# Kernel optimization log

Hardware: AMD Instinct MI355X
Metric: run time of the kernel (lower is better)

Reference implementation:

```python
import jax, jax.numpy as jnp
import numpy as np

N = 100_000      # nodes
E = 3_200_000    # edges (avg degree 32)
G = 1024         # graphs in batch
IN_FEAT = 6
H_FEAT = 64
NUM_TARGETS = 2
NEG_SLOPE = 0.01


def setup_inputs() -> dict:
    key = jax.random.key(0)
    ks = jax.random.split(key, 9)
    x = jax.random.normal(ks[0], (N, IN_FEAT), jnp.float32)
    edge_index = jax.random.randint(ks[1], (2, E), 0, N, dtype=jnp.int64)
    batch = jnp.sort(jax.random.randint(ks[2], (N,), 0, G, dtype=jnp.int64))
    W1 = jax.random.normal(ks[3], (IN_FEAT, H_FEAT), jnp.float32) / np.sqrt(IN_FEAT)
    b1 = jnp.zeros((H_FEAT,), jnp.float32)
    W2 = jax.random.normal(ks[4], (H_FEAT, H_FEAT // 2), jnp.float32) / np.sqrt(H_FEAT)
    b2 = jnp.zeros((H_FEAT // 2,), jnp.float32)
    Wlin = jax.random.normal(ks[5], (H_FEAT // 2, NUM_TARGETS), jnp.float32) / np.sqrt(H_FEAT // 2)
    blin = jnp.zeros((NUM_TARGETS,), jnp.float32)
    return {"x": x, "edge_index": edge_index, "batch": batch,
            "W1": W1, "b1": b1, "W2": W2, "b2": b2, "Wlin": Wlin, "blin": blin}


def _gcn_conv(x, W, b, src, dst, dis):
    # GCNConv: linear transform, then symmetric-normalized scatter-add.
    h = x @ W                                   # [N, out]
    norm = dis[src] * dis[dst]                  # [E+N]
    msg = h[src] * norm[:, None]                # gather + scale
    out = jax.ops.segment_sum(msg, dst, num_segments=N)
    return out + b


def reference(x, edge_index, batch, W1, b1, W2, b2, Wlin, blin):
    loop = jnp.arange(N, dtype=edge_index.dtype)
    src = jnp.concatenate([edge_index[0], loop])   # add self-loops
    dst = jnp.concatenate([edge_index[1], loop])
    deg = jax.ops.segment_sum(jnp.ones_like(dst, dtype=x.dtype), dst, num_segments=N)
    dis = jax.lax.rsqrt(jnp.maximum(deg, 1.0))     # deg >= 1 via self-loops

    h = jax.nn.leaky_relu(_gcn_conv(x, W1, b1, src, dst, dis), NEG_SLOPE)
    h = jax.nn.leaky_relu(_gcn_conv(h, W2, b2, src, dst, dis), NEG_SLOPE)

    # global_mean_pool over graph ids
    sums = jax.ops.segment_sum(h, batch, num_segments=G)              # [G, 32]
    cnt = jax.ops.segment_sum(jnp.ones((N,), h.dtype), batch, num_segments=G)
    pooled = sums / jnp.maximum(cnt, 1.0)[:, None]

    # dropout(p=0.5) is identity in eval mode
    return pooled @ Wlin + blin                                        # [G, 2]
```

## Files before the change

### kernel.cpp

```cpp
#include <hip/hip_runtime.h>


#define N_NODES 100000
#define N_EDGES 3200000
#define N_GRAPHS 1024
#define IN_F 6
#define H1 64
#define H2 32
#define SLOPE 0.01f

#define NBIN 400
#define BIN_N 250
#define CAP2 8704
#define CAP2R 10752

#define SEG 8192
#define NSEGB ((N_EDGES + SEG - 1) / SEG)

typedef _Float16 f16;
typedef _Float16 h2 __attribute__((ext_vector_type(2)));
typedef float f2 __attribute__((ext_vector_type(2)));
typedef int  iv4 __attribute__((ext_vector_type(4)));

static __device__ __forceinline__ float lrelu(float v) {
    return v > 0.0f ? v : SLOPE * v;
}

static __device__ __forceinline__ h2 uph(unsigned w) {
    union { unsigned u; h2 h; } cv; cv.u = w;
    return cv.h;
}

static __device__ __forceinline__ void upk8(unsigned w, f2& lo, f2& hi) {
    lo = __builtin_amdgcn_cvt_pk_f32_fp8((int)w, false);
    hi = __builtin_amdgcn_cvt_pk_f32_fp8((int)w, true);
}

static __device__ __forceinline__ unsigned pk8(float a, float b, float c, float d) {
    int v = __builtin_amdgcn_cvt_pk_fp8_f32(a, b, 0, false);
    v = __builtin_amdgcn_cvt_pk_fp8_f32(c, d, v, true);
    return (unsigned)v;
}

__global__ void k_init(float* __restrict__ gz, int* __restrict__ bz,
                       unsigned* __restrict__ t2z, f16* __restrict__ sxz) {
    int i = blockIdx.x * blockDim.x + threadIdx.x;
    if (i < N_GRAPHS * H2 + N_GRAPHS) gz[i] = 0.0f;
    if (i < NBIN + 16) bz[i] = 0;
    if (i < 8) t2z[i] = 0u;
    if (i < 8) sxz[i] = (f16)0.0f;
}

__global__ void k_bin400(const int* __restrict__ src, const int* __restrict__ dst,
                         int* __restrict__ bcur2, unsigned* __restrict__ benc2) {
    __shared__ int hist[NBIN];
    __shared__ int lscan[NBIN];
    __shared__ int lcur[NBIN];
    __shared__ int gbase[NBIN];
    __shared__ int scn[512];
    __shared__ unsigned codes[SEG];
    __shared__ unsigned short bslot[SEG];
    int tid = threadIdx.x;
    for (int i = tid; i < NBIN; i += 256) hist[i] = 0;
    __syncthreads();
    int e0 = blockIdx.x * SEG;
    int e1 = e0 + SEG; if (e1 > N_EDGES) e1 = N_EDGES;
    int cnt = e1 - e0;
    const iv4* d4 = (const iv4*)dst;
    const iv4* s4 = (const iv4*)src;
    int i40 = e0 >> 2, i41 = e1 >> 2;
    for (int i4 = i40 + tid; i4 < i41; i4 += 256) {
        iv4 v = __builtin_nontemporal_load(d4 + i4);
        atomicAdd(&hist[v.x / BIN_N], 1);
        atomicAdd(&hist[v.y / BIN_N], 1);
        atomicAdd(&hist[v.z / BIN_N], 1);
        atomicAdd(&hist[v.w / BIN_N], 1);
    }
    __syncthreads();
    scn[tid]       = (tid < NBIN) ? hist[tid] : 0;
    scn[tid + 256] = (tid + 256 < NBIN) ? hist[tid + 256] : 0;
    __syncthreads();
    for (int off = 1; off < 512; off <<= 1) {
        int v0 = (tid >= off) ? scn[tid - off] : 0;
        int v1 = (tid + 256 >= off) ? scn[tid + 256 - off] : 0;
        __syncthreads();
        scn[tid] += v0;
        scn[tid + 256] += v1;
        __syncthreads();
    }
    if (tid < NBIN) {
        int h = hist[tid];
        int ls = scn[tid] - h;
        lscan[tid] = ls;
        lcur[tid] = ls;
        gbase[tid] = h ? atomicAdd(&bcur2[tid], h) : 0;
        for (int j = ls; j < ls + h; ++j) bslot[j] = (unsigned short)tid;
    }
    if (tid + 256 < NBIN) {
        int t = tid + 256;
        int h = hist[t];
        int ls = scn[t] - h;
        lscan[t] = ls;
        lcur[t] = ls;
        gbase[t] = h ? atomicAdd(&bcur2[t], h) : 0;
        for (int j = ls; j < ls + h; ++j) bslot[j] = (unsigned short)t;
    }
    __syncthreads();
    for (int i4 = i40 + tid; i4 < i41; i4 += 256) {
        iv4 dv = __builtin_nontemporal_load(d4 + i4);
        iv4 sv = __builtin_nontemporal_load(s4 + i4);
        int b, p;
        b = dv.x / BIN_N; p = atomicAdd(&lcur[b], 1);
        codes[p] = ((unsigned)sv.x << 8) | (unsigned)(dv.x - b * BIN_N);
        b = dv.y / BIN_N; p = atomicAdd(&lcur[b], 1);
        codes[p] = ((unsigned)sv.y << 8) | (unsigned)(dv.y - b * BIN_N);
        b = dv.z / BIN_N; p = atomicAdd(&lcur[b], 1);
        codes[p] = ((unsigned)sv.z << 8) | (unsigned)(dv.z - b * BIN_N);
        b = dv.w / BIN_N; p = atomicAdd(&lcur[b], 1);
        codes[p] = ((unsigned)sv.w << 8) | (unsigned)(dv.w - b * BIN_N);
    }
    __syncthreads();
    for (int slot = tid; slot < cnt; slot += 256) {
        int b = bslot[slot];
        int g = gbase[b] + (slot - lscan[b]);
        benc2[(long long)b * CAP2 + g] = codes[slot];
    }
}

__global__ void k_sort(const unsigned* __restrict__ benc2, const int* __restrict__ bcur2,
                       const float* __restrict__ x,
                       int* __restrict__ csr, int* __restrict__ obeg, int* __restrict__ oend,
                       float* __restrict__ dis, f16* __restrict__ sx) {
    __shared__ int hist[256];
    __shared__ int scn[256];
    __shared__ int lcur[256];
    int bin = blockIdx.x;
    int tid = threadIdx.x;
    hist[tid] = 0;
    __syncthreads();
    int cnt = bcur2[bin];
    const unsigned* p = benc2 + (long long)bin * CAP2;
    for (int i = tid; i < cnt; i += 256)
        atomicAdd(&hist[p[i] & 0xFFu], 1);
    __syncthreads();
    int deg = hist[tid];
    int pad = (deg + 7) & ~7;
    scn[tid] = pad;
    __syncthreads();
    for (int off = 1; off < 256; off <<= 1) {
        int v = 0;
        if (tid >= off) v = scn[tid - off];
        __syncthreads();
        if (tid >= off) scn[tid] += v;
        __syncthreads();
    }
    int excl = scn[tid] - pad;
    int gbase = bin * CAP2R;
    lcur[tid] = gbase + excl;
    if (tid < BIN_N) {
        int n = bin * BIN_N + tid;
        obeg[n] = gbase + excl;
        oend[n] = gbase + excl + pad;
        float dn = rsqrtf((float)(deg + 1));
        dis[n] = dn;
#pragma unroll
        for (int j = 0; j < IN_F; ++j)
            sx[n * 8 + j] = (f16)(x[n * IN_F + j] * dn);
        sx[n * 8 + 6] = (f16)0.0f;
        sx[n * 8 + 7] = (f16)0.0f;
    }
    __syncthreads();
    for (int i = tid; i < cnt; i += 256) {
        unsigned c = p[i];
        int pos = atomicAdd(&lcur[c & 0xFFu], 1);
        csr[pos] = (int)(c >> 8);
    }
    __syncthreads();
    if (tid < BIN_N) {
        int end = gbase + excl + pad;
        for (int j = lcur[tid]; j < end; ++j) csr[j] = N_NODES;
    }
}

__global__ void k_l1(const unsigned* __restrict__ sxu, const int* __restrict__ obeg,
                     const int* __restrict__ oend, const int* __restrict__ csr,
                     const float* __restrict__ W1, const float* __restrict__ b1,
                     const float* __restrict__ W2, const float* __restrict__ dis,
                     unsigned* __restrict__ t2) {
    __shared__ float sW1[IN_F * H1];
    __shared__ float sb1[H1];
    __shared__ float sW2[H1 * H2];
    __shared__ float sagg[64][9];
    __shared__ float sh1[64][H1 + 1];
    __shared__ float sdis[64];
    int tid = threadIdx.x;
    for (int i = tid; i < IN_F * H1; i += 256) sW1[i] = W1[i];
    if (tid < H1) sb1[tid] = b1[tid];
    for (int i = tid; i < H1 * H2; i += 256) sW2[i] = W2[i];
    int loc = tid >> 2;
    int f = tid & 3;
    int n = blockIdx.x * 64 + loc;
    bool ok = n < N_NODES;
    if (ok) {
        h2 acc = uph(sxu[(n << 2) + f]);
        int b = obeg[n], e = oend[n];
        for (int j = b; j < e; j += 8) {
            const iv4* p = (const iv4*)(csr + j);
            iv4 ia = p[0], ib = p[1];
            unsigned w[8];
            w[0] = sxu[(ia.x << 2) + f]; w[1] = sxu[(ia.y << 2) + f];
            w[2] = sxu[(ia.z << 2) + f]; w[3] = sxu[(ia.w << 2) + f];
            w[4] = sxu[(ib.x << 2) + f]; w[5] = sxu[(ib.y << 2) + f];
            w[6] = sxu[(ib.z << 2) + f]; w[7] = sxu[(ib.w << 2) + f];
            h2 s01 = uph(w[0]) + uph(w[1]);
            h2 s23 = uph(w[2]) + uph(w[3]);
            h2 s45 = uph(w[4]) + uph(w[5]);
            h2 s67 = uph(w[6]) + uph(w[7]);
            acc += (s01 + s23) + (s45 + s67);
        }
        sagg[loc][2*f]   = (float)acc.x;
        sagg[loc][2*f+1] = (float)acc.y;
        if (f == 0) sdis[loc] = dis[n];
    }
    __syncthreads();
    float dn = sdis[loc];
#pragma unroll
    for (int q = 0; q < 16; ++q) {
        int k = (f << 4) + q;
        float s = 0.0f;
#pragma unroll
        for (int j = 0; j < IN_F; ++j) s += sagg[loc][j] * sW1[j * H1 + k];
        sh1[loc][k] = lrelu(s * dn + sb1[k]);
    }
    __syncthreads();
    float r[8];
#pragma unroll
    for (int q = 0; q < 8; ++q) {
        int f2i = (f << 3) + q;
        float s = 0.0f;
#pragma unroll
        for (int k = 0; k < H1; ++k) s += sh1[loc][k] * sW2[k * H2 + f2i];
        r[q] = s * dn;
    }
    if (ok) {
        uint2 pk;
        pk.x = pk8(r[0], r[1], r[2], r[3]);
        pk.y = pk8(r[4], r[5], r[6], r[7]);
        *((uint2*)(t2 + n * 8 + f * 2)) = pk;
    }
}

__global__ void k_gather2(const unsigned* __restrict__ t2u, const int* __restrict__ obeg,
                          const int* __restrict__ oend, const int* __restrict__ csr,
                          const float* __restrict__ dis, const float* __restrict__ b2,
                          const int* __restrict__ batch,
                          float* __restrict__ gsum, float* __restrict__ gcnt) {
    __shared__ float sv[32][H2];
    __shared__ int sg[32];
    int idx = blockIdx.x * blockDim.x + threadIdx.x;
    int n = idx >> 3;
    int f = idx & 7;
    f2 a01, a23;
    upk8(t2u[(n << 3) + f], a01, a23);
    int b = obeg[n], e = oend[n];
    int j = b;
    for (; j + 16 <= e; j += 16) {
        const iv4* p = (const iv4*)(csr + j);
        iv4 ia = p[0], ib = p[1], ic = p[2], id = p[3];
        unsigned w[16];
        w[0]  = t2u[(ia.x << 3) + f]; w[1]  = t2u[(ia.y << 3) + f];
        w[2]  = t2u[(ia.z << 3) + f]; w[3]  = t2u[(ia.w << 3) + f];
        w[4]  = t2u[(ib.x << 3) + f]; w[5]  = t2u[(ib.y << 3) + f];
        w[6]  = t2u[(ib.z << 3) + f]; w[7]  = t2u[(ib.w << 3) + f];
        w[8]  = t2u[(ic.x << 3) + f]; w[9]  = t2u[(ic.y << 3) + f];
        w[10] = t2u[(ic.z << 3) + f]; w[11] = t2u[(ic.w << 3) + f];
        w[12] = t2u[(id.x << 3) + f]; w[13] = t2u[(id.y << 3) + f];
        w[14] = t2u[(id.z << 3) + f]; w[15] = t2u[(id.w << 3) + f];
#pragma unroll
        for (int q = 0; q < 16; ++q) {
            f2 lo, hi;
            upk8(w[q], lo, hi);
            a01 += lo;
            a23 += hi;
        }
    }
    if (j < e) {
        const iv4* p = (const iv4*)(csr + j);
        iv4 ia = p[0], ib = p[1];
        unsigned w[8];
        w[0] = t2u[(ia.x << 3) + f]; w[1] = t2u[(ia.y << 3) + f];
        w[2] = t2u[(ia.z << 3) + f]; w[3] = t2u[(ia.w << 3) + f];
        w[4] = t2u[(ib.x << 3) + f]; w[5] = t2u[(ib.y << 3) + f];
        w[6] = t2u[(ib.z << 3) + f]; w[7] = t2u[(ib.w << 3) + f];
#pragma unroll
        for (int q = 0; q < 8; ++q) {
            f2 lo, hi;
            upk8(w[q], lo, hi);
            a01 += lo;
            a23 += hi;
        }
    }
    float dn = dis[n];
    float v0 = lrelu(a01.x * dn + b2[4*f]);
    float v1 = lrelu(a01.y * dn + b2[4*f+1]);
    float v2 = lrelu(a23.x * dn + b2[4*f+2]);
    float v3 = lrelu(a23.y * dn + b2[4*f+3]);
    int g = batch[n];
    int loc = threadIdx.x >> 3;
    sv[loc][4*f]   = v0;
    sv[loc][4*f+1] = v1;
    sv[loc][4*f+2] = v2;
    sv[loc][4*f+3] = v3;
    if (f == 0) sg[loc] = g;
    __syncthreads();
    bool leader = true;
    for (int l = 0; l < loc; ++l) leader &= (sg[l] != g);
    if (leader) {
        float s0 = v0, s1 = v1, s2 = v2, s3 = v3;
        float c = 1.0f;
        for (int l = loc + 1; l < 32; ++l)
            if (sg[l] == g) {
                s0 += sv[l][4*f];   s1 += sv[l][4*f+1];
                s2 += sv[l][4*f+2]; s3 += sv[l][4*f+3];
                c += 1.0f;
            }
        atomicAdd(&gsum[g * H2 + 4*f],     s0);
        atomicAdd(&gsum[g * H2 + 4*f + 1], s1);
        atomicAdd(&gsum[g * H2 + 4*f + 2], s2);
        atomicAdd(&gsum[g * H2 + 4*f + 3], s3);
        if (f == 0) atomicAdd(&gcnt[g], c);
    }
}

__global__ void k_final(const float* __restrict__ gsum, const float* __restrict__ gcnt,
                        const float* __restrict__ Wlin, const float* __restrict__ blin,
                        float* __restrict__ out) {
    int idx = blockIdx.x * blockDim.x + threadIdx.x;
    if (idx >= N_GRAPHS * 2) return;
    int g = idx >> 1;
    int t = idx & 1;
    float inv = 1.0f / fmaxf(gcnt[g], 1.0f);
    float s = blin[t];
#pragma unroll
    for (int ff = 0; ff < H2; ++ff)
        s += gsum[g * H2 + ff] * inv * Wlin[ff * 2 + t];
    out[idx] = s;
}

static inline int cdiv(long long a, int b) { return (int)((a + b - 1) / b); }

extern "C" void kernel_launch(void* const* d_in, const int* in_sizes, int n_in,
                              void* d_out, int out_size, void* d_ws, size_t ws_size,
                              hipStream_t stream) {
    const float* x    = (const float*)d_in[0];
    const int*   ei   = (const int*)d_in[1];
    const int*   batch= (const int*)d_in[2];
    const float* W1   = (const float*)d_in[3];
    const float* b1   = (const float*)d_in[4];
    const float* W2   = (const float*)d_in[5];
    const float* b2   = (const float*)d_in[6];
    const float* Wlin = (const float*)d_in[7];
    const float* blin = (const float*)d_in[8];
    float* out = (float*)d_out;

    const int* src = ei;
    const int* dst = ei + N_EDGES;

    unsigned* t2 = (unsigned*)d_ws;
    f16*   sx   = (f16*)(t2 + 8LL * (N_NODES + 1));
    float* dis  = (float*)(sx + 8LL * (N_NODES + 1));
    float* gsum = dis + N_NODES;
    float* gcnt = gsum + (long long)N_GRAPHS * H2;
    size_t ioff = ((size_t)(gcnt + N_GRAPHS) + 15) & ~(size_t)15;
    int*  bcur2   = (int*)ioff;
    int*  obeg    = bcur2 + NBIN + 16;
    int*  oend    = obeg + N_NODES;
    unsigned* benc2 = (unsigned*)(oend + N_NODES);
    int*  csr      = (int*)(benc2 + (long long)NBIN * CAP2);

    const int B = 256;

    k_init<<<cdiv(N_GRAPHS * H2 + N_GRAPHS, B), B, 0, stream>>>(
        gsum, bcur2, t2 + 8LL * N_NODES, sx + 8LL * N_NODES);

    k_bin400<<<NSEGB, B, 0, stream>>>(src, dst, bcur2, benc2);
    k_sort<<<NBIN, B, 0, stream>>>(benc2, bcur2, x, csr, obeg, oend, dis, sx);

    k_l1<<<cdiv(N_NODES, 64), B, 0, stream>>>((const unsigned*)sx, obeg, oend, csr,
                                              W1, b1, W2, dis, t2);
    k_gather2<<<cdiv((long long)N_NODES * 8, B), B, 0, stream>>>(
        (const unsigned*)t2, obeg, oend, csr, dis, b2, batch, gsum, gcnt);
    k_final<<<cdiv(N_GRAPHS * 2, B), B, 0, stream>>>(gsum, gcnt, Wlin, blin, out);
}
```

Before: 128.9 us.

## Partition bin buffers per XCD to localize atomics and writes

The binning kernel now reads the hardware XCC id and keeps a separate set of bin counters and bin buffers for each of the 8 XCDs. This avoids cross-XCD contention on the global atomic counters and keeps the scattered writes local to one die. The sort kernel then walks all 8 sub-buckets for its bin. The cost is more, smaller segments to read, and the per-XCD capacity of 3072 could overflow if the distribution of blocks across XCDs is skewed.

After: 118.2 us. -8.3%, faster.

```diff
diff --git a/kernel.cpp b/kernel.cpp
--- a/kernel.cpp
+++ b/kernel.cpp
@@ -11,11 +11,14 @@
 
 #define NBIN 400
 #define BIN_N 250
-#define CAP2 8704
+#define NXCD 8
+#define CAP2X 3072
 #define CAP2R 10752
 
 #define SEG 8192
 #define NSEGB ((N_EDGES + SEG - 1) / SEG)
+
+#define XCC_ID_REG 14356
 
 typedef _Float16 f16;
 typedef _Float16 h2 __attribute__((ext_vector_type(2)));
@@ -46,7 +49,7 @@
                        unsigned* __restrict__ t2z, f16* __restrict__ sxz) {
     int i = blockIdx.x * blockDim.x + threadIdx.x;
     if (i < N_GRAPHS * H2 + N_GRAPHS) gz[i] = 0.0f;
-    if (i < NBIN + 16) bz[i] = 0;
+    if (i < NXCD * NBIN + 16) bz[i] = 0;
     if (i < 8) t2z[i] = 0u;
     if (i < 8) sxz[i] = (f16)0.0f;
 }
@@ -61,6 +64,9 @@
     __shared__ unsigned codes[SEG];
     __shared__ unsigned short bslot[SEG];
     int tid = threadIdx.x;
+    int xcd = __builtin_amdgcn_s_getreg(XCC_ID_REG) & (NXCD - 1);
+    int* mycur = bcur2 + xcd * NBIN;
+    unsigned* myenc = benc2 + (long long)xcd * NBIN * CAP2X;
     for (int i = tid; i < NBIN; i += 256) hist[i] = 0;
     __syncthreads();
     int e0 = blockIdx.x * SEG;
@@ -93,7 +99,7 @@
         int ls = scn[tid] - h;
         lscan[tid] = ls;
         lcur[tid] = ls;
-        gbase[tid] = h ? atomicAdd(&bcur2[tid], h) : 0;
+        gbase[tid] = h ? atomicAdd(&mycur[tid], h) : 0;
         for (int j = ls; j < ls + h; ++j) bslot[j] = (unsigned short)tid;
     }
     if (tid + 256 < NBIN) {
@@ -102,7 +108,7 @@
         int ls = scn[t] - h;
         lscan[t] = ls;
         lcur[t] = ls;
-        gbase[t] = h ? atomicAdd(&bcur2[t], h) : 0;
+        gbase[t] = h ? atomicAdd(&mycur[t], h) : 0;
         for (int j = ls; j < ls + h; ++j) bslot[j] = (unsigned short)t;
     }
     __syncthreads();
@@ -123,7 +129,7 @@
     for (int slot = tid; slot < cnt; slot += 256) {
         int b = bslot[slot];
         int g = gbase[b] + (slot - lscan[b]);
-        benc2[(long long)b * CAP2 + g] = codes[slot];
+        myenc[(long long)b * CAP2X + g] = codes[slot];
     }
 }
 
@@ -138,10 +144,12 @@
     int tid = threadIdx.x;
     hist[tid] = 0;
     __syncthreads();
-    int cnt = bcur2[bin];
-    const unsigned* p = benc2 + (long long)bin * CAP2;
-    for (int i = tid; i < cnt; i += 256)
-        atomicAdd(&hist[p[i] & 0xFFu], 1);
+    for (int xc = 0; xc < NXCD; ++xc) {
+        int cnt = bcur2[xc * NBIN + bin];
+        const unsigned* p = benc2 + ((long long)xc * NBIN + bin) * CAP2X;
+        for (int i = tid; i < cnt; i += 256)
+            atomicAdd(&hist[p[i] & 0xFFu], 1);
+    }
     __syncthreads();
     int deg = hist[tid];
     int pad = (deg + 7) & ~7;
@@ -170,10 +178,14 @@
         sx[n * 8 + 7] = (f16)0.0f;
     }
     __syncthreads();
-    for (int i = tid; i < cnt; i += 256) {
-        unsigned c = p[i];
-        int pos = atomicAdd(&lcur[c & 0xFFu], 1);
-        csr[pos] = (int)(c >> 8);
+    for (int xc = 0; xc < NXCD; ++xc) {
+        int cnt = bcur2[xc * NBIN + bin];
+        const unsigned* p = benc2 + ((long long)xc * NBIN + bin) * CAP2X;
+        for (int i = tid; i < cnt; i += 256) {
+            unsigned c = p[i];
+            int pos = atomicAdd(&lcur[c & 0xFFu], 1);
+            csr[pos] = (int)(c >> 8);
+        }
     }
     __syncthreads();
     if (tid < BIN_N) {
@@ -371,12 +383,13 @@
     float* dis  = (float*)(sx + 8LL * (N_NODES + 1));
     float* gsum = dis + N_NODES;
     float* gcnt = gsum + (long long)N_GRAPHS * H2;
-    size_t ioff = ((size_t)(gcnt + N_GRAPHS) + 15) & ~(size_t)15;
+    size_t ioff = ((size_t)(gcnt + N_GRAPHS) + 63) & ~(size_t)63;
     int*  bcur2   = (int*)ioff;
-    int*  obeg    = bcur2 + NBIN + 16;
+    int*  obeg    = bcur2 + NXCD * NBIN + 16;
     int*  oend    = obeg + N_NODES;
-    unsigned* benc2 = (unsigned*)(oend + N_NODES);
-    int*  csr      = (int*)(benc2 + (long long)NBIN * CAP2);
+    size_t boff = ((size_t)(oend + N_NODES) + 63) & ~(size_t)63;
+    unsigned* benc2 = (unsigned*)boff;
+    int*  csr      = (int*)(benc2 + (long long)NXCD * NBIN * CAP2X);
 
     const int B = 256;
 
```
